# Kernel tuning notes

Hardware: AMD Instinct MI355X
Metric: run time of the kernel (lower is better)

Reference implementation:

```python
import jax, jax.numpy as jnp
import numpy as np

NBINS = 30
EMBED = 300


def setup_inputs() -> dict:
    key = jax.random.key(0)
    ks = jax.random.split(key, 12)
    B, Q, D = 64, 32, 4096
    inp = {
        "query": jax.random.normal(ks[0], (B, Q, EMBED), dtype=jnp.float32),
        "document": jax.random.normal(ks[1], (B, D, EMBED), dtype=jnp.float32),
        "query_len": jax.random.randint(ks[2], (B,), 0, Q, dtype=jnp.int32),
        # ffn: Linear(30,5) -> Tanh -> Linear(5,1) -> Tanh -> Linear(1,1) -> Tanh
        "W1": jax.random.normal(ks[3], (5, NBINS), dtype=jnp.float32) * 0.1,
        "b1": jax.random.normal(ks[4], (5,), dtype=jnp.float32) * 0.1,
        "W2": jax.random.normal(ks[5], (1, 5), dtype=jnp.float32) * 0.1,
        "b2": jax.random.normal(ks[6], (1,), dtype=jnp.float32) * 0.1,
        "W3": jax.random.normal(ks[7], (1, 1), dtype=jnp.float32) * 0.1,
        "b3": jax.random.normal(ks[8], (1,), dtype=jnp.float32) * 0.1,
        # gate: Linear(embed_dim, 1)
        "Wg": jax.random.normal(ks[9], (1, EMBED), dtype=jnp.float32) * 0.05,
        "bg": jax.random.normal(ks[10], (1,), dtype=jnp.float32) * 0.05,
    }
    return inp


def _batched_hist(interaction, mask, dtype):
    # interaction: [B, Q, D] cosine sims in [-1, 1]; mask: [B, Q] bool (q < query_len)
    B, Q, D = interaction.shape
    # torch.histc(bins=NBINS, min=-1, max=1): bin = floor((x+1)*NBINS/2), clip top edge
    idx = jnp.clip(jnp.floor((interaction + 1.0) * (NBINS / 2.0)).astype(jnp.int32), 0, NBINS - 1)
    row = jnp.arange(B * Q, dtype=jnp.int32)[:, None]  # [B*Q, 1]
    flat = (row * NBINS + idx.reshape(B * Q, D)).reshape(-1)
    counts = jax.ops.segment_sum(jnp.ones((B * Q * D,), dtype=dtype), flat,
                                 num_segments=B * Q * NBINS)
    counts = counts.reshape(B, Q, NBINS)
    # rows with q >= query_len[b] stay zero in the torch code
    return counts * mask[..., None].astype(dtype)


def reference(query, document, query_len, W1, b1, W2, b2, W3, b3, Wg, bg):
    B, Q, E = query.shape
    qn = query / jnp.linalg.norm(query, axis=2, keepdims=True)
    dn = document / jnp.linalg.norm(document, axis=2, keepdims=True)
    interaction = jnp.einsum('bqe,bde->bqd', qn, dn)  # [B, Q, D]
    mask = jnp.arange(Q, dtype=jnp.int32)[None, :] < query_len[:, None]  # [B, Q]
    h = jnp.log1p(_batched_hist(interaction, mask, query.dtype))  # [B, Q, NBINS]
    z = jnp.tanh(h @ W1.T + b1)
    z = jnp.tanh(z @ W2.T + b2)
    z = jnp.tanh(z @ W3.T + b3)[..., 0]  # [B, Q]
    g = jax.nn.softmax((qn @ Wg.T + bg)[..., 0], axis=1)  # note: torch gates on normalized query
    return jnp.sum(z * g, axis=1)  # [B]
```

## Files before the change

kernel.cpp:

```cpp
#include <hip/hip_runtime.h>
#include <math.h>

#define BB 64
#define QQ 32
#define DD 4096
#define EE 300
#define EPAD 320
#define NB 30
#define TDB 128
#define NDT (DD/TDB)
#define KC 32
#define NCH 10

typedef __attribute__((ext_vector_type(8))) short short8v;
typedef __attribute__((ext_vector_type(4))) float f32x4;

static __device__ __forceinline__ unsigned short f2bf(float x) {
    unsigned int u = __builtin_bit_cast(unsigned int, x);
    u = (u + 0x7FFFu + ((u >> 16) & 1u)) >> 16;
    return (unsigned short)u;
}
static __device__ __forceinline__ float bf2f(unsigned short h) {
    return __builtin_bit_cast(float, (unsigned int)h << 16);
}

__global__ __launch_bounds__(64) void drmm_prep(const float* __restrict__ query,
                                                const float* __restrict__ Wg,
                                                const float* __restrict__ bg,
                                                unsigned short* __restrict__ qh,
                                                unsigned short* __restrict__ ql,
                                                float* __restrict__ glog,
                                                int* __restrict__ ghist) {
    const int row  = blockIdx.x;
    const int lane = threadIdx.x;
    if (lane < NB) ghist[(size_t)row * NB + lane] = 0;
    const float* src = query + (size_t)row * EE;
    float ss = 0.f;
    for (int e = lane; e < EE; e += 64) { float x = src[e]; ss += x * x; }
    for (int o = 1; o < 64; o <<= 1) ss += __shfl_xor(ss, o);
    const float inv = 1.0f / sqrtf(ss);
    float gd = 0.f;
    #pragma unroll
    for (int it = 0; it < 5; ++it) {
        int e = it * 64 + lane;
        float x = (e < EE) ? src[e] * inv : 0.f;
        unsigned short h = f2bf(x);
        float lo = x - bf2f(h);
        qh[(size_t)row * EPAD + e] = h;
        ql[(size_t)row * EPAD + e] = f2bf(lo);
        if (e < EE) gd += x * Wg[e];
    }
    for (int o = 1; o < 64; o <<= 1) gd += __shfl_xor(gd, o);
    if (lane == 0) glog[row] = gd + bg[0];
}

__global__ __launch_bounds__(256, 4) void drmm_main(const float* __restrict__ doc,
                                                    const int* __restrict__ qlen,
                                                    const unsigned short* __restrict__ qh,
                                                    const unsigned short* __restrict__ ql,
                                                    int* __restrict__ ghist) {
    __shared__ __align__(16) float s_doc[2][TDB * KC];
    __shared__ __align__(16) unsigned short s_qh[2][QQ * KC];
    __shared__ __align__(16) unsigned short s_ql[2][QQ * KC];

    const int b   = blockIdx.x >> 5;
    const int dt  = blockIdx.x & 31;
    const int len = __builtin_amdgcn_readfirstlane(qlen[b]);
    if (len == 0) return;

    const int tid = threadIdx.x;
    const int wv  = tid >> 6;
    const int td  = tid & 63;
    const int l15 = tid & 15;
    const int l4  = (tid >> 4) & 3;
    const int nqt = (len > 16) ? 2 : 1;

    const float* docb = doc + ((size_t)b * DD + dt * TDB) * EE;
    const unsigned short* qhb = qh + (size_t)b * QQ * EPAD;
    const unsigned short* qlb = ql + (size_t)b * QQ * EPAD;

    auto STAGE = [&](int c, int buf) {
        #pragma unroll
        for (int i = 0; i < 4; ++i) {
            int S  = i * 256 + tid;
            int r  = S >> 3;
            int lg = (S & 7) ^ (r & 7);
            int kk = c * KC + 4 * lg;
            if (kk >= EE) kk = 0;
            __builtin_amdgcn_global_load_lds(
                (const __attribute__((address_space(1))) void*)(docb + (size_t)r * EE + kk),
                (__attribute__((address_space(3))) void*)&s_doc[buf][(i * 256 + wv * 64) * 4],
                16, 0, 0);
        }
        if (wv < 2) {
            int s  = wv * 64 + td;
            int q  = s >> 2;
            int lg = (s & 3) ^ (q & 3);
            __builtin_amdgcn_global_load_lds(
                (const __attribute__((address_space(1))) void*)
                    (qhb + (size_t)q * EPAD + c * KC + 8 * lg),
                (__attribute__((address_space(3))) void*)&s_qh[buf][wv * 512],
                16, 0, 0);
        } else {
            int s  = (wv - 2) * 64 + td;
            int q  = s >> 2;
            int lg = (s & 3) ^ (q & 3);
            __builtin_amdgcn_global_load_lds(
                (const __attribute__((address_space(1))) void*)
                    (qlb + (size_t)q * EPAD + c * KC + 8 * lg),
                (__attribute__((address_space(3))) void*)&s_ql[buf][(wv - 2) * 512],
                16, 0, 0);
        }
    };

    STAGE(0, 0);

    f32x4 acc[2][2];
    #pragma unroll
    for (int qt = 0; qt < 2; ++qt)
        #pragma unroll
        for (int t = 0; t < 2; ++t) acc[qt][t] = (f32x4){0.f, 0.f, 0.f, 0.f};
    float ssq[2] = {0.f, 0.f};

    int cur = 0;
    for (int c = 0; c < NCH; ++c) {
        if (c + 1 < NCH) {
            STAGE(c + 1, cur ^ 1);
            asm volatile("s_waitcnt vmcnt(5)" ::: "memory");
        } else {
            asm volatile("s_waitcnt vmcnt(0)" ::: "memory");
        }
        __builtin_amdgcn_s_barrier();

        short8v ah[2], al[2];
        #pragma unroll
        for (int qt = 0; qt < 2; ++qt) {
            if (qt < nqt) {
                const int qrow = qt * 16 + l15;
                const int p = l4 ^ (qrow & 3);
                ah[qt] = *(const short8v*)&s_qh[cur][qrow * KC + p * 8];
                al[qt] = *(const short8v*)&s_ql[cur][qrow * KC + p * 8];
            }
        }

        const int kb = c * KC + l4 * 8;
        const bool r1 = (kb < EE), r2 = (kb + 4 < EE);

        #pragma unroll
        for (int t = 0; t < 2; ++t) {
            const int lrow = wv * 32 + t * 16 + l15;
            const int p0 = (2 * l4)     ^ (lrow & 7);
            const int p1 = (2 * l4 + 1) ^ (lrow & 7);
            const f32x4 v0 = *(const f32x4*)&s_doc[cur][lrow * KC + p0 * 4];
            const f32x4 v1 = *(const f32x4*)&s_doc[cur][lrow * KC + p1 * 4];
            if (r1) ssq[t] += v0.x * v0.x + v0.y * v0.y + v0.z * v0.z + v0.w * v0.w;
            if (r2) ssq[t] += v1.x * v1.x + v1.y * v1.y + v1.z * v1.z + v1.w * v1.w;

            short8v bhi, blo;
            #pragma unroll
            for (int j = 0; j < 4; ++j) {
                unsigned short h0 = f2bf(v0[j]);
                unsigned short h1 = f2bf(v1[j]);
                bhi[j]     = (short)h0;
                bhi[j + 4] = (short)h1;
                blo[j]     = (short)f2bf(v0[j] - bf2f(h0));
                blo[j + 4] = (short)f2bf(v1[j] - bf2f(h1));
            }
            acc[0][t] = __builtin_amdgcn_mfma_f32_16x16x32_bf16(ah[0], bhi, acc[0][t], 0, 0, 0);
            acc[0][t] = __builtin_amdgcn_mfma_f32_16x16x32_bf16(ah[0], blo, acc[0][t], 0, 0, 0);
            acc[0][t] = __builtin_amdgcn_mfma_f32_16x16x32_bf16(al[0], bhi, acc[0][t], 0, 0, 0);
            if (nqt > 1) {
                acc[1][t] = __builtin_amdgcn_mfma_f32_16x16x32_bf16(ah[1], bhi, acc[1][t], 0, 0, 0);
                acc[1][t] = __builtin_amdgcn_mfma_f32_16x16x32_bf16(ah[1], blo, acc[1][t], 0, 0, 0);
                acc[1][t] = __builtin_amdgcn_mfma_f32_16x16x32_bf16(al[1], bhi, acc[1][t], 0, 0, 0);
            }
        }
        __builtin_amdgcn_s_barrier();
        cur ^= 1;
    }

    float rinv[2];
    #pragma unroll
    for (int t = 0; t < 2; ++t) {
        float s = ssq[t];
        s += __shfl_xor(s, 16);
        s += __shfl_xor(s, 32);
        rinv[t] = 1.0f / sqrtf(s);
    }

    int* hist = (int*)&s_doc[0][0];
    for (int s = tid; s < QQ * 32; s += 256) hist[s] = 0;
    __syncthreads();

    #pragma unroll
    for (int qt = 0; qt < 2; ++qt) {
        #pragma unroll
        for (int r = 0; r < 4; ++r) {
            const int q = qt * 16 + l4 * 4 + r;
            if (q < len) {
                #pragma unroll
                for (int t = 0; t < 2; ++t) {
                    float sim = acc[qt][t][r] * rinv[t];
                    int bin = (int)floorf((sim + 1.0f) * 15.0f);
                    bin = bin < 0 ? 0 : (bin > 29 ? 29 : bin);
                    atomicAdd(&hist[q * 32 + bin], 1);
                }
            }
        }
    }
    __syncthreads();

    for (int s = tid; s < QQ * NB; s += 256) {
        const int q = s / NB, bin = s % NB;
        int tot = hist[q * 32 + bin];
        if (tot) atomicAdd(&ghist[((size_t)b * QQ + q) * NB + bin], tot);
    }
}

__global__ __launch_bounds__(64) void drmm_final(const int* __restrict__ ghist,
                                                 const float* __restrict__ glog,
                                                 const float* __restrict__ W1,
                                                 const float* __restrict__ b1,
                                                 const float* __restrict__ W2,
                                                 const float* __restrict__ b2,
                                                 const float* __restrict__ W3,
                                                 const float* __restrict__ b3,
                                                 float* __restrict__ out) {
    const int b = blockIdx.x;
    const int lane = threadIdx.x;
    float z = 0.f, lg = -1e30f;
    if (lane < QQ) {
        const int* hrow = ghist + ((size_t)b * QQ + lane) * NB;
        float h[NB];
        #pragma unroll
        for (int v = 0; v < NB; ++v) h[v] = log1pf((float)hrow[v]);
        float t1[5];
        #pragma unroll
        for (int u = 0; u < 5; ++u) {
            float s = b1[u];
            #pragma unroll
            for (int v = 0; v < NB; ++v) s += W1[u * NB + v] * h[v];
            t1[u] = tanhf(s);
        }
        float s2 = b2[0];
        #pragma unroll
        for (int u = 0; u < 5; ++u) s2 += W2[u] * t1[u];
        z = tanhf(W3[0] * tanhf(s2) + b3[0]);
        lg = glog[b * QQ + lane];
    }
    float m = lg;
    for (int o = 16; o >= 1; o >>= 1) m = fmaxf(m, __shfl_xor(m, o));
    float e = (lane < QQ) ? expf(lg - m) : 0.f;
    float s = e;
    for (int o = 16; o >= 1; o >>= 1) s += __shfl_xor(s, o);
    float w = z * (e / s);
    for (int o = 16; o >= 1; o >>= 1) w += __shfl_xor(w, o);
    if (lane == 0) out[b] = w;
}

extern "C" void kernel_launch(void* const* d_in, const int* in_sizes, int n_in,
                              void* d_out, int out_size, void* d_ws, size_t ws_size,
                              hipStream_t stream) {
    const float* query = (const float*)d_in[0];
    const float* doc   = (const float*)d_in[1];
    const int*   qlen  = (const int*)d_in[2];
    const float* W1    = (const float*)d_in[3];
    const float* b1    = (const float*)d_in[4];
    const float* W2    = (const float*)d_in[5];
    const float* b2    = (const float*)d_in[6];
    const float* W3    = (const float*)d_in[7];
    const float* b3    = (const float*)d_in[8];
    const float* Wg    = (const float*)d_in[9];
    const float* bg    = (const float*)d_in[10];
    float* out = (float*)d_out;

    unsigned short* qh = (unsigned short*)d_ws;
    unsigned short* ql = qh + (size_t)BB * QQ * EPAD;
    float* glog = (float*)(ql + (size_t)BB * QQ * EPAD);
    int*   hist = (int*)(glog + BB * QQ);

    hipLaunchKernelGGL(drmm_prep, dim3(BB * QQ), dim3(64), 0, stream,
                       query, Wg, bg, qh, ql, glog, hist);
    hipLaunchKernelGGL(drmm_main, dim3(BB * NDT), dim3(256), 0, stream,
                       doc, qlen, qh, ql, hist);
    hipLaunchKernelGGL(drmm_final, dim3(BB), dim3(64), 0, stream,
                       hist, glog, W1, b1, W2, b2, W3, b3, out);
}
```

Baseline: 94.90 us.

## Load query fragments directly into registers instead of staging through LDS

Query hi/lo bf16 fragments are now read straight from global memory into registers, each lane fetching its own 8-element slice, instead of being copied into LDS via global_load_lds and read back. The main loop is unrolled by two with ping-pong register sets for the query fragments, and the wait counts are adjusted to cover the extra outstanding loads. Dropping the LDS query buffers lowers shared memory use, and launch bounds are raised to 5 blocks per CU to aim for higher occupancy. In exchange, register pressure goes up and the query data is loaded with uncoalesced per-lane global reads that now rely on the caches for reuse.

```diff
diff --git a/kernel.cpp b/kernel.cpp
--- a/kernel.cpp
+++ b/kernel.cpp
@@ -54,14 +54,12 @@
     if (lane == 0) glog[row] = gd + bg[0];
 }
 
-__global__ __launch_bounds__(256, 4) void drmm_main(const float* __restrict__ doc,
+__global__ __launch_bounds__(256, 5) void drmm_main(const float* __restrict__ doc,
                                                     const int* __restrict__ qlen,
                                                     const unsigned short* __restrict__ qh,
                                                     const unsigned short* __restrict__ ql,
                                                     int* __restrict__ ghist) {
     __shared__ __align__(16) float s_doc[2][TDB * KC];
-    __shared__ __align__(16) unsigned short s_qh[2][QQ * KC];
-    __shared__ __align__(16) unsigned short s_ql[2][QQ * KC];
 
     const int b   = blockIdx.x >> 5;
     const int dt  = blockIdx.x & 31;
@@ -70,14 +68,13 @@
 
     const int tid = threadIdx.x;
     const int wv  = tid >> 6;
-    const int td  = tid & 63;
     const int l15 = tid & 15;
     const int l4  = (tid >> 4) & 3;
     const int nqt = (len > 16) ? 2 : 1;
 
     const float* docb = doc + ((size_t)b * DD + dt * TDB) * EE;
-    const unsigned short* qhb = qh + (size_t)b * QQ * EPAD;
-    const unsigned short* qlb = ql + (size_t)b * QQ * EPAD;
+    const unsigned short* qhb = qh + ((size_t)b * QQ + l15) * EPAD + l4 * 8;
+    const unsigned short* qlb = ql + ((size_t)b * QQ + l15) * EPAD + l4 * 8;
 
     auto STAGE = [&](int c, int buf) {
         #pragma unroll
@@ -92,28 +89,15 @@
                 (__attribute__((address_space(3))) void*)&s_doc[buf][(i * 256 + wv * 64) * 4],
                 16, 0, 0);
         }
-        if (wv < 2) {
-            int s  = wv * 64 + td;
-            int q  = s >> 2;
-            int lg = (s & 3) ^ (q & 3);
-            __builtin_amdgcn_global_load_lds(
-                (const __attribute__((address_space(1))) void*)
-                    (qhb + (size_t)q * EPAD + c * KC + 8 * lg),
-                (__attribute__((address_space(3))) void*)&s_qh[buf][wv * 512],
-                16, 0, 0);
-        } else {
-            int s  = (wv - 2) * 64 + td;
-            int q  = s >> 2;
-            int lg = (s & 3) ^ (q & 3);
-            __builtin_amdgcn_global_load_lds(
-                (const __attribute__((address_space(1))) void*)
-                    (qlb + (size_t)q * EPAD + c * KC + 8 * lg),
-                (__attribute__((address_space(3))) void*)&s_ql[buf][(wv - 2) * 512],
-                16, 0, 0);
-        }
     };
-
-    STAGE(0, 0);
+    auto LOADQ = [&](int c, short8v (&ah)[2], short8v (&al)[2]) {
+        ah[0] = *(const short8v*)(qhb + c * KC);
+        al[0] = *(const short8v*)(qlb + c * KC);
+        if (nqt > 1) {
+            ah[1] = *(const short8v*)(qhb + 16 * EPAD + c * KC);
+            al[1] = *(const short8v*)(qlb + 16 * EPAD + c * KC);
+        }
+    };
 
     f32x4 acc[2][2];
     #pragma unroll
@@ -122,37 +106,16 @@
         for (int t = 0; t < 2; ++t) acc[qt][t] = (f32x4){0.f, 0.f, 0.f, 0.f};
     float ssq[2] = {0.f, 0.f};
 
-    int cur = 0;
-    for (int c = 0; c < NCH; ++c) {
-        if (c + 1 < NCH) {
-            STAGE(c + 1, cur ^ 1);
-            asm volatile("s_waitcnt vmcnt(5)" ::: "memory");
-        } else {
-            asm volatile("s_waitcnt vmcnt(0)" ::: "memory");
-        }
-        __builtin_amdgcn_s_barrier();
-
-        short8v ah[2], al[2];
-        #pragma unroll
-        for (int qt = 0; qt < 2; ++qt) {
-            if (qt < nqt) {
-                const int qrow = qt * 16 + l15;
-                const int p = l4 ^ (qrow & 3);
-                ah[qt] = *(const short8v*)&s_qh[cur][qrow * KC + p * 8];
-                al[qt] = *(const short8v*)&s_ql[cur][qrow * KC + p * 8];
-            }
-        }
-
+    auto BODY = [&](int c, int buf, const short8v (&ah)[2], const short8v (&al)[2]) {
         const int kb = c * KC + l4 * 8;
         const bool r1 = (kb < EE), r2 = (kb + 4 < EE);
-
         #pragma unroll
         for (int t = 0; t < 2; ++t) {
             const int lrow = wv * 32 + t * 16 + l15;
             const int p0 = (2 * l4)     ^ (lrow & 7);
             const int p1 = (2 * l4 + 1) ^ (lrow & 7);
-            const f32x4 v0 = *(const f32x4*)&s_doc[cur][lrow * KC + p0 * 4];
-            const f32x4 v1 = *(const f32x4*)&s_doc[cur][lrow * KC + p1 * 4];
+            const f32x4 v0 = *(const f32x4*)&s_doc[buf][lrow * KC + p0 * 4];
+            const f32x4 v1 = *(const f32x4*)&s_doc[buf][lrow * KC + p1 * 4];
             if (r1) ssq[t] += v0.x * v0.x + v0.y * v0.y + v0.z * v0.z + v0.w * v0.w;
             if (r2) ssq[t] += v1.x * v1.x + v1.y * v1.y + v1.z * v1.z + v1.w * v1.w;
 
@@ -175,8 +138,37 @@
                 acc[1][t] = __builtin_amdgcn_mfma_f32_16x16x32_bf16(al[1], bhi, acc[1][t], 0, 0, 0);
             }
         }
-        __builtin_amdgcn_s_barrier();
-        cur ^= 1;
+    };
+
+    short8v qAh[2], qAl[2], qBh[2], qBl[2];
+    LOADQ(0, qAh, qAl);
+    STAGE(0, 0);
+
+    #pragma unroll
+    for (int cc = 0; cc < NCH; cc += 2) {
+        if (cc + 1 < NCH) {
+            LOADQ(cc + 1, qBh, qBl);
+            STAGE(cc + 1, 1);
+            if (nqt > 1) asm volatile("s_waitcnt vmcnt(8)" ::: "memory");
+            else         asm volatile("s_waitcnt vmcnt(6)" ::: "memory");
+        } else {
+            asm volatile("s_waitcnt vmcnt(0)" ::: "memory");
+        }
+        __builtin_amdgcn_s_barrier();
+        BODY(cc, 0, qAh, qAl);
+        __builtin_amdgcn_s_barrier();
+
+        if (cc + 2 < NCH) {
+            LOADQ(cc + 2, qAh, qAl);
+            STAGE(cc + 2, 0);
+            if (nqt > 1) asm volatile("s_waitcnt vmcnt(8)" ::: "memory");
+            else         asm volatile("s_waitcnt vmcnt(6)" ::: "memory");
+        } else {
+            asm volatile("s_waitcnt vmcnt(0)" ::: "memory");
+        }
+        __builtin_amdgcn_s_barrier();
+        BODY(cc + 1, 1, qBh, qBl);
+        __builtin_amdgcn_s_barrier();
     }
 
     float rinv[2];
```

Result: slower. 244.1 us (+157.2%).
